# Performance work log

Measured on AMD Instinct MI355X. Metric: run time of the kernel, lower is better.

The kernel has to match this reference:

```python
import jax, jax.numpy as jnp
import numpy as np

B, S, W = 16, 512, 5
H, E, V = 512, 256, 100000


def setup_inputs() -> dict:
    key = jax.random.key(0)
    ks = jax.random.split(key, 20)
    inp = {
        "hiddens": jax.random.normal(ks[0], (B, S, H), jnp.float32),
        "masks": jax.random.randint(ks[1], (B, S), 0, 2, jnp.int32),
        "begins": jax.random.randint(ks[2], (B, S, W), 0, V, jnp.int32),
        "begin_lens": jax.random.randint(ks[3], (B, S), 0, W + 1, jnp.int32),
        "middles": jax.random.randint(ks[4], (B, S, W), 0, V, jnp.int32),
        "middle_lens": jax.random.randint(ks[5], (B, S), 0, W + 1, jnp.int32),
        "ends": jax.random.randint(ks[6], (B, S, W), 0, V, jnp.int32),
        "end_lens": jax.random.randint(ks[7], (B, S), 0, W + 1, jnp.int32),
        # parameters
        "emb": jax.random.normal(ks[8], (V, E), jnp.float32) * 0.02,
        "W_hidden": jax.random.normal(ks[9], (H, 3 * H), jnp.float32) * (1.0 / np.sqrt(H)),
        "b_hidden": jnp.zeros((3 * H,), jnp.float32),
        "W_begin": jax.random.normal(ks[10], (E, 2 * H), jnp.float32) * (1.0 / np.sqrt(E)),
        "b_begin": jnp.zeros((2 * H,), jnp.float32),
        "W_middle": jax.random.normal(ks[11], (E, 2 * H), jnp.float32) * (1.0 / np.sqrt(E)),
        "b_middle": jnp.zeros((2 * H,), jnp.float32),
        "W_end": jax.random.normal(ks[12], (E, 2 * H), jnp.float32) * (1.0 / np.sqrt(E)),
        "b_end": jnp.zeros((2 * H,), jnp.float32),
        "W_gate": jax.random.normal(ks[13], (H, 9), jnp.float32) * (1.0 / np.sqrt(H)),
        "b_gate": jnp.zeros((9,), jnp.float32),
    }
    return inp


def _len_mask(lens, w):
    # True where the lattice candidate is valid (mimics _make_mask's 1s)
    return jnp.arange(w)[None, None, :] < lens[:, :, None]


def _gates(hiddens, masks, W_gate, b_gate):
    b, s, _ = hiddens.shape
    lmr = hiddens @ W_gate + b_gate                      # (B,S,9)
    left, mid, right = jnp.split(lmr, 3, axis=-1)        # each (B,S,3)
    g = jax.nn.sigmoid(left[:, :-2] + mid[:, 1:-1] + right[:, 2:])  # (B,S-2,3)
    ones = jnp.ones((b, 1), g.dtype)
    zeros = jnp.zeros((b, 1), g.dtype)
    begin_g = jnp.concatenate([ones, g[..., 0], ones], axis=1)
    mid_g = jnp.concatenate([zeros, g[..., 1], zeros], axis=1)
    end_g = jnp.concatenate([ones, g[..., 2], ones], axis=1)
    pad = masks == 0
    z = jnp.zeros((), g.dtype)
    return (jnp.where(pad, z, begin_g), jnp.where(pad, z, mid_g), jnp.where(pad, z, end_g))


def reference(hiddens, masks, begins, begin_lens, middles, middle_lens, ends, end_lens,
              emb, W_hidden, b_hidden, W_begin, b_begin, W_middle, b_middle,
              W_end, b_end, W_gate, b_gate):
    w = begins.shape[-1]
    begin_m = _len_mask(begin_lens, w)
    middle_m = _len_mask(middle_lens, w)
    end_m = _len_mask(end_lens, w)

    begin_kv = emb[begins] @ W_begin + b_begin           # (B,S,W,2H)
    middle_kv = emb[middles] @ W_middle + b_middle
    end_kv = emb[ends] @ W_end + b_end

    query, hidden_key, hidden_value = jnp.split(hiddens @ W_hidden + b_hidden, 3, axis=-1)
    bg, mg, eg = _gates(hiddens, masks, W_gate, b_gate)
    begin_kv = bg[:, :, None, None] * begin_kv
    middle_kv = mg[:, :, None, None] * middle_kv
    end_kv = eg[:, :, None, None] * end_kv

    kv = jnp.concatenate([begin_kv, middle_kv, end_kv], axis=-2)   # (B,S,3W,2H)
    h = hiddens.shape[-1]
    keys, values = jnp.split(kv, 2, axis=-1)
    keys = jnp.concatenate([hidden_key[:, :, None, :], keys], axis=-2)     # (B,S,1+3W,H)
    values = jnp.concatenate([hidden_value[:, :, None, :], values], axis=-2)

    # combined mask: True entries get -1e10 (faithful to masked_fill_(masks, -1e10))
    score_mask = jnp.concatenate(
        [(masks != 0)[:, :, None], begin_m, middle_m, end_m], axis=-1)     # (B,S,1+3W)

    scores = jnp.einsum("bsh,bskh->bsk", query, keys)
    scores = jnp.where(score_mask, jnp.asarray(-1e10, scores.dtype), scores)
    weights = jax.nn.softmax(scores, axis=-1)
    return jnp.einsum("bsk,bskh->bsh", weights, values)
```

## Files before the change

kernel.cpp:

```cpp
#include <hip/hip_runtime.h>
#include <cstdint>
#include <cstddef>


typedef unsigned short u16;
typedef __attribute__((ext_vector_type(8))) short short8;
typedef __attribute__((ext_vector_type(8))) __bf16 bf16x8;
typedef __attribute__((ext_vector_type(4))) float f32x4;

#define MROWS 8192
#define SS 512

static __device__ __forceinline__ u16 f2bf(float x) {
  uint32_t u = __builtin_bit_cast(uint32_t, x);
  u += 0x7FFFu + ((u >> 16) & 1u);
  return (u16)(u >> 16);
}
static __device__ __forceinline__ float bf2f(u16 h) {
  return __builtin_bit_cast(float, (uint32_t)h << 16);
}
static __device__ __forceinline__ float sigm(float x) { return 1.f / (1.f + __expf(-x)); }

static __device__ __forceinline__ void gl2lds(const u16* g, u16* l) {
  __builtin_amdgcn_global_load_lds(
      (const __attribute__((address_space(1))) unsigned int*)g,
      (__attribute__((address_space(3))) unsigned int*)l, 16, 0, 0);
}

__global__ __launch_bounds__(256) void prep_xlmr(
    const float* __restrict__ X, const float* __restrict__ Wg,
    const float* __restrict__ bg, u16* __restrict__ hi, u16* __restrict__ lo,
    float* __restrict__ lmr) {
  __shared__ float wg[4608];
  const int t = threadIdx.x;
  for (int i = t; i < 4608; i += 256) wg[i] = Wg[i];
  __syncthreads();
  const int lane = t & 63, wid = t >> 6;
#pragma unroll
  for (int it = 0; it < 4; it++) {
    int pos = blockIdx.x * 16 + it * 4 + wid;
    const float* x = X + (size_t)pos * 512 + lane * 8;
    float4 x0 = *(const float4*)x;
    float4 x1 = *(const float4*)(x + 4);
    float xs[8] = {x0.x, x0.y, x0.z, x0.w, x1.x, x1.y, x1.z, x1.w};
    ushort4 h0, h1, l0, l1;
    h0.x = f2bf(xs[0]); l0.x = f2bf(xs[0] - bf2f(h0.x));
    h0.y = f2bf(xs[1]); l0.y = f2bf(xs[1] - bf2f(h0.y));
    h0.z = f2bf(xs[2]); l0.z = f2bf(xs[2] - bf2f(h0.z));
    h0.w = f2bf(xs[3]); l0.w = f2bf(xs[3] - bf2f(h0.w));
    h1.x = f2bf(xs[4]); l1.x = f2bf(xs[4] - bf2f(h1.x));
    h1.y = f2bf(xs[5]); l1.y = f2bf(xs[5] - bf2f(h1.y));
    h1.z = f2bf(xs[6]); l1.z = f2bf(xs[6] - bf2f(h1.z));
    h1.w = f2bf(xs[7]); l1.w = f2bf(xs[7] - bf2f(h1.w));
    ((ushort4*)hi)[pos * 128 + lane * 2] = h0;
    ((ushort4*)hi)[pos * 128 + lane * 2 + 1] = h1;
    ((ushort4*)lo)[pos * 128 + lane * 2] = l0;
    ((ushort4*)lo)[pos * 128 + lane * 2 + 1] = l1;
    float p[9];
#pragma unroll
    for (int c = 0; c < 9; c++) p[c] = 0.f;
    const float* wrow = wg + (lane * 8) * 9;
#pragma unroll
    for (int j = 0; j < 8; j++)
#pragma unroll
      for (int c = 0; c < 9; c++) p[c] += xs[j] * wrow[j * 9 + c];
#pragma unroll
    for (int c = 0; c < 9; c++)
#pragma unroll
      for (int o = 32; o > 0; o >>= 1) p[c] += __shfl_xor(p[c], o);
    if (lane == 0) {
#pragma unroll
      for (int c = 0; c < 9; c++) lmr[(size_t)pos * 9 + c] = p[c] + bg[c];
    }
  }
}

__global__ __launch_bounds__(256) void prep_weights(
    const float* __restrict__ Wh, const float* __restrict__ Wb,
    const float* __restrict__ Wm, const float* __restrict__ We,
    const float* __restrict__ bb, const float* __restrict__ bm,
    const float* __restrict__ be, const float* __restrict__ lmr,
    const int* __restrict__ masks, u16* __restrict__ WhThi,
    u16* __restrict__ WhTlo, u16* __restrict__ WkT, u16* __restrict__ WvT,
    float* __restrict__ gates) {
  __shared__ float tile[64][65];
  const int b = blockIdx.x;
  const int t = threadIdx.x;
  if (b < 192) {
    int k0 = (b & 7) * 64;
    int n0 = (b >> 3) * 64;
#pragma unroll
    for (int i = 0; i < 16; i++) {
      int li = i * 256 + t; int r = li >> 6, c = li & 63;
      tile[r][c] = Wh[(size_t)(k0 + r) * 1536 + n0 + c];
    }
    __syncthreads();
#pragma unroll
    for (int i = 0; i < 16; i++) {
      int li = i * 256 + t; int r = li >> 6, c = li & 63;
      float v = tile[c][r];
      size_t o = (size_t)(n0 + r) * 512 + k0 + c;
      u16 h = f2bf(v);
      WhThi[o] = h;
      WhTlo[o] = f2bf(v - bf2f(h));
    }
  } else if (b < 640) {
    int tid = (b - 192) * 256 + t;
    int n = tid >> 7;
    int kq = (tid & 127) * 4;
    float4 v;
    if (n < 768) {
      int ty = n >> 8, c = n & 255;
      const float* src = (ty == 0 ? Wb : ty == 1 ? Wm : We) + (size_t)c * 1024 + kq;
      v = *(const float4*)src;
    } else if (n < 771) {
      int ty = n - 768;
      const float* src = (ty == 0 ? bb : ty == 1 ? bm : be) + kq;
      v = *(const float4*)src;
    } else {
      v = make_float4(0.f, 0.f, 0.f, 0.f);
    }
    ushort4 h; h.x = f2bf(v.x); h.y = f2bf(v.y); h.z = f2bf(v.z); h.w = f2bf(v.w);
    ((ushort4*)WkT)[tid] = h;
  } else if (b < 736) {
    int idx = b - 640;
    int ty = idx >> 5;
    int rem = idx & 31;
    int c0 = (rem & 3) * 64;
    int n0 = (rem >> 2) * 64;
    const float* Wsrc = ty == 0 ? Wb : ty == 1 ? Wm : We;
#pragma unroll
    for (int i = 0; i < 16; i++) {
      int li = i * 256 + t; int r = li >> 6, c = li & 63;
      tile[r][c] = Wsrc[(size_t)(c0 + r) * 1024 + 512 + n0 + c];
    }
    __syncthreads();
#pragma unroll
    for (int i = 0; i < 16; i++) {
      int li = i * 256 + t; int r = li >> 6, c = li & 63;
      WvT[(size_t)(n0 + r) * 768 + ty * 256 + c0 + c] = f2bf(tile[c][r]);
    }
  } else {
    int pos = (b - 736) * 256 + t;
    int s = pos & (SS - 1);
    float g0, g1, g2;
    if (masks[pos] == 0) {
      g0 = g1 = g2 = 0.f;
    } else if (s == 0 || s == SS - 1) {
      g0 = 1.f; g1 = 0.f; g2 = 1.f;
    } else {
      const float* p0 = lmr + (size_t)(pos - 1) * 9;
      const float* p1 = lmr + (size_t)pos * 9;
      const float* p2 = lmr + (size_t)(pos + 1) * 9;
      g0 = sigm(p0[0] + p1[3] + p2[6]);
      g1 = sigm(p0[1] + p1[4] + p2[7]);
      g2 = sigm(p0[2] + p1[5] + p2[8]);
    }
    gates[(size_t)pos * 3 + 0] = g0;
    gates[(size_t)pos * 3 + 1] = g1;
    gates[(size_t)pos * 3 + 2] = g2;
  }
}

template <bool MAYSPLIT, bool ADDOUT, bool WRITE_QBF, bool HAS_BIAS, bool OUTBF>
__global__ __launch_bounds__(256) void gemm_mfma(
    const u16* __restrict__ Ahi, const u16* __restrict__ Alo,
    const u16* __restrict__ Bhi, const u16* __restrict__ Blo,
    const float* __restrict__ bias, float* __restrict__ Cf, u16* __restrict__ Cb,
    u16* __restrict__ Qbf, int Kdim, int ldC, int splitN) {
  __shared__ __align__(16) u16 As_hi[128 * 32];
  __shared__ __align__(16) u16 Bs_hi[128 * 32];
  __shared__ __align__(16) u16 As_lo[MAYSPLIT ? 128 * 32 : 8];
  __shared__ __align__(16) u16 Bs_lo[MAYSPLIT ? 128 * 32 : 8];

  const int t = threadIdx.x;
  const int lane = t & 63;
  const int wid = t >> 6;
  const int m0 = blockIdx.x * 128;
  const int n0 = blockIdx.y * 128;
  const bool split = MAYSPLIT && (n0 < splitN);
  const int wm = (wid & 1) * 64;
  const int wn = (wid >> 1) * 64;
  const int fr = lane & 15;
  const int kq = (lane >> 4) * 8;

  f32x4 acc[4][4];
#pragma unroll
  for (int i = 0; i < 4; i++)
#pragma unroll
    for (int j = 0; j < 4; j++) acc[i][j] = (f32x4){0.f, 0.f, 0.f, 0.f};

  for (int k0 = 0; k0 < Kdim; k0 += 32) {
    __syncthreads();
#pragma unroll
    for (int p = 0; p < 2; p++) {
      int li = p * 256 + t;
      int row = li >> 2;
      int so = (li & 3) * 8;
      size_t ga = (size_t)(m0 + row) * Kdim + k0 + so;
      size_t gb = (size_t)(n0 + row) * Kdim + k0 + so;
      int ls = li * 8;
      gl2lds(&Ahi[ga], &As_hi[ls]);
      gl2lds(&Bhi[gb], &Bs_hi[ls]);
      if (MAYSPLIT && split) {
        gl2lds(&Alo[ga], &As_lo[ls]);
        gl2lds(&Blo[gb], &Bs_lo[ls]);
      }
    }
    __syncthreads();
    short8 ah[4], bh[4], al[4], bl[4];
#pragma unroll
    for (int i = 0; i < 4; i++) {
      ah[i] = *(const short8*)&As_hi[(wm + i * 16 + fr) * 32 + kq];
      bh[i] = *(const short8*)&Bs_hi[(wn + i * 16 + fr) * 32 + kq];
      if (MAYSPLIT && split) {
        al[i] = *(const short8*)&As_lo[(wm + i * 16 + fr) * 32 + kq];
        bl[i] = *(const short8*)&Bs_lo[(wn + i * 16 + fr) * 32 + kq];
      }
    }
#pragma unroll
    for (int mt = 0; mt < 4; mt++)
#pragma unroll
      for (int nt = 0; nt < 4; nt++) {
        acc[mt][nt] = __builtin_amdgcn_mfma_f32_16x16x32_bf16(
            __builtin_bit_cast(bf16x8, ah[mt]), __builtin_bit_cast(bf16x8, bh[nt]),
            acc[mt][nt], 0, 0, 0);
        if (MAYSPLIT && split) {
          acc[mt][nt] = __builtin_amdgcn_mfma_f32_16x16x32_bf16(
              __builtin_bit_cast(bf16x8, al[mt]), __builtin_bit_cast(bf16x8, bh[nt]),
              acc[mt][nt], 0, 0, 0);
          acc[mt][nt] = __builtin_amdgcn_mfma_f32_16x16x32_bf16(
              __builtin_bit_cast(bf16x8, ah[mt]), __builtin_bit_cast(bf16x8, bl[nt]),
              acc[mt][nt], 0, 0, 0);
        }
      }
  }

  const int r0 = (lane >> 4) * 4;
#pragma unroll
  for (int mt = 0; mt < 4; mt++) {
#pragma unroll
    for (int nt = 0; nt < 4; nt++) {
      int col = n0 + wn + nt * 16 + fr;
      float bv = 0.f;
      if constexpr (HAS_BIAS) bv = bias[col];
#pragma unroll
      for (int r = 0; r < 4; r++) {
        int row = m0 + wm + mt * 16 + r0 + r;
        size_t off = (size_t)row * ldC + col;
        float v = acc[mt][nt][r] + bv;
        if constexpr (ADDOUT) v += Cf[off];
        if constexpr (OUTBF) Cb[off] = f2bf(v);
        else Cf[off] = v;
        if constexpr (WRITE_QBF) {
          if (col < 512) Qbf[(size_t)row * 512 + col] = f2bf(v);
        }
      }
    }
  }
}

__global__ __launch_bounds__(256) void attn_kernel(
    const int* __restrict__ masks, const int* __restrict__ begins,
    const int* __restrict__ blens, const int* __restrict__ middles,
    const int* __restrict__ mlens, const int* __restrict__ ends,
    const int* __restrict__ elens, const float* __restrict__ emb,
    const float* __restrict__ QKV, const u16* __restrict__ Pb,
    const float* __restrict__ gates, const float* __restrict__ b_begin,
    const float* __restrict__ b_middle, const float* __restrict__ b_end,
    float* __restrict__ out, u16* __restrict__ Ebar) {
  __shared__ float bvs[3][512];
  {
    int tt = threadIdx.x;
    for (int i = tt; i < 512; i += 256) {
      bvs[0][i] = b_begin[512 + i];
      bvs[1][i] = b_middle[512 + i];
      bvs[2][i] = b_end[512 + i];
    }
  }
  __syncthreads();
  const int t = threadIdx.x;
  const int lane = t & 63;
  const int wid = t >> 6;
  const int pos = blockIdx.x * 4 + wid;
  const int mask = masks[pos];
  const float* qkv = QKV + (size_t)pos * 1536;
  float4 hv0 = *(const float4*)(qkv + 1024 + lane * 8);
  float4 hv1 = *(const float4*)(qkv + 1024 + lane * 8 + 4);
  float* orow = out + (size_t)pos * 512;
  u16* erow = Ebar + (size_t)pos * 768;

  if (mask == 0) {
    float4 q0 = *(const float4*)(qkv + lane * 8);
    float4 q1 = *(const float4*)(qkv + lane * 8 + 4);
    float4 k0 = *(const float4*)(qkv + 512 + lane * 8);
    float4 k1 = *(const float4*)(qkv + 512 + lane * 8 + 4);
    float p = q0.x * k0.x + q0.y * k0.y + q0.z * k0.z + q0.w * k0.w +
              q1.x * k1.x + q1.y * k1.y + q1.z * k1.z + q1.w * k1.w;
#pragma unroll
    for (int o = 32; o > 0; o >>= 1) p += __shfl_xor(p, o);
    float s0 = p;
    int nv = min(blens[pos], 5) + min(mlens[pos], 5) + min(elens[pos], 5);
    int ninv = 15 - nv;
    float w0;
    if (ninv == 0) {
      w0 = 1.f;
    } else {
      float Mx = fmaxf(s0, 0.f);
      float e0 = __expf(s0 - Mx);
      w0 = e0 / (e0 + (float)ninv * __expf(-Mx));
    }
    float4 o0, o1;
    o0.x = w0 * hv0.x; o0.y = w0 * hv0.y; o0.z = w0 * hv0.z; o0.w = w0 * hv0.w;
    o1.x = w0 * hv1.x; o1.y = w0 * hv1.y; o1.z = w0 * hv1.z; o1.w = w0 * hv1.w;
    *(float4*)(orow + lane * 8) = o0;
    *(float4*)(orow + lane * 8 + 4) = o1;
    ushort4 zz; zz.x = zz.y = zz.z = zz.w = 0;
    *(ushort4*)(erow + 0 * 256 + lane * 4) = zz;
    *(ushort4*)(erow + 1 * 256 + lane * 4) = zz;
    *(ushort4*)(erow + 2 * 256 + lane * 4) = zz;
  } else {
    float g[3];
    g[0] = gates[(size_t)pos * 3 + 0];
    g[1] = gates[(size_t)pos * 3 + 1];
    g[2] = gates[(size_t)pos * 3 + 2];
    const u16* prow = Pb + (size_t)pos * 896;
    float4 Pt[3];
    float qb[3];
#pragma unroll
    for (int ty = 0; ty < 3; ty++) {
      ushort4 pu = *(const ushort4*)(prow + ty * 256 + lane * 4);
      Pt[ty].x = bf2f(pu.x); Pt[ty].y = bf2f(pu.y);
      Pt[ty].z = bf2f(pu.z); Pt[ty].w = bf2f(pu.w);
      qb[ty] = bf2f(prow[768 + ty]);
    }
    int lens[3] = {blens[pos], mlens[pos], elens[pos]};
    const int* ib = begins + (size_t)pos * 5;
    const int* im = middles + (size_t)pos * 5;
    const int* ie = ends + (size_t)pos * 5;
    float4 ev[3][5];
#pragma unroll
    for (int w = 0; w < 5; w++) {
      ev[0][w] = *(const float4*)(emb + (size_t)ib[w] * 256 + lane * 4);
      ev[1][w] = *(const float4*)(emb + (size_t)im[w] * 256 + lane * 4);
      ev[2][w] = *(const float4*)(emb + (size_t)ie[w] * 256 + lane * 4);
    }
    float sc[16];
    sc[0] = -1e10f;
#pragma unroll
    for (int ty = 0; ty < 3; ty++) {
#pragma unroll
      for (int w = 0; w < 5; w++) {
        float4 e = ev[ty][w];
        float d = Pt[ty].x * e.x + Pt[ty].y * e.y + Pt[ty].z * e.z + Pt[ty].w * e.w;
#pragma unroll
        for (int o = 32; o > 0; o >>= 1) d += __shfl_xor(d, o);
        sc[1 + ty * 5 + w] = (w < lens[ty]) ? -1e10f : g[ty] * (d + qb[ty]);
      }
    }
    float Mx = sc[0];
#pragma unroll
    for (int k = 1; k < 16; k++) Mx = fmaxf(Mx, sc[k]);
    float wts[16];
    float zs = 0.f;
#pragma unroll
    for (int k = 0; k < 16; k++) {
      wts[k] = __expf(sc[k] - Mx);
      zs += wts[k];
    }
    float inv = 1.f / zs;
    float alpha[3];
#pragma unroll
    for (int ty = 0; ty < 3; ty++) {
      float ax = 0.f, ay = 0.f, az = 0.f, aw = 0.f, asum = 0.f;
#pragma unroll
      for (int w = 0; w < 5; w++) {
        float wk = wts[1 + ty * 5 + w];
        asum += wk;
        ax += wk * ev[ty][w].x;
        ay += wk * ev[ty][w].y;
        az += wk * ev[ty][w].z;
        aw += wk * ev[ty][w].w;
      }
      float sg = g[ty] * inv;
      alpha[ty] = sg * asum;
      ushort4 h;
      h.x = f2bf(ax * sg); h.y = f2bf(ay * sg); h.z = f2bf(az * sg); h.w = f2bf(aw * sg);
      *(ushort4*)(erow + ty * 256 + lane * 4) = h;
    }
    float w0 = wts[0] * inv;
    float4 o0, o1;
    int hb = lane * 8;
    o0.x = w0 * hv0.x + alpha[0] * bvs[0][hb + 0] + alpha[1] * bvs[1][hb + 0] + alpha[2] * bvs[2][hb + 0];
    o0.y = w0 * hv0.y + alpha[0] * bvs[0][hb + 1] + alpha[1] * bvs[1][hb + 1] + alpha[2] * bvs[2][hb + 1];
    o0.z = w0 * hv0.z + alpha[0] * bvs[0][hb + 2] + alpha[1] * bvs[1][hb + 2] + alpha[2] * bvs[2][hb + 2];
    o0.w = w0 * hv0.w + alpha[0] * bvs[0][hb + 3] + alpha[1] * bvs[1][hb + 3] + alpha[2] * bvs[2][hb + 3];
    o1.x = w0 * hv1.x + alpha[0] * bvs[0][hb + 4] + alpha[1] * bvs[1][hb + 4] + alpha[2] * bvs[2][hb + 4];
    o1.y = w0 * hv1.y + alpha[0] * bvs[0][hb + 5] + alpha[1] * bvs[1][hb + 5] + alpha[2] * bvs[2][hb + 5];
    o1.z = w0 * hv1.z + alpha[0] * bvs[0][hb + 6] + alpha[1] * bvs[1][hb + 6] + alpha[2] * bvs[2][hb + 6];
    o1.w = w0 * hv1.w + alpha[0] * bvs[0][hb + 7] + alpha[1] * bvs[1][hb + 7] + alpha[2] * bvs[2][hb + 7];
    *(float4*)(orow + lane * 8) = o0;
    *(float4*)(orow + lane * 8 + 4) = o1;
  }
}

extern "C" void kernel_launch(void* const* d_in, const int* in_sizes, int n_in,
                              void* d_out, int out_size, void* d_ws, size_t ws_size,
                              hipStream_t stream) {
  const float* hiddens = (const float*)d_in[0];
  const int* masks = (const int*)d_in[1];
  const int* begins = (const int*)d_in[2];
  const int* blens = (const int*)d_in[3];
  const int* middles = (const int*)d_in[4];
  const int* mlens = (const int*)d_in[5];
  const int* ends = (const int*)d_in[6];
  const int* elens = (const int*)d_in[7];
  const float* emb = (const float*)d_in[8];
  const float* Wh = (const float*)d_in[9];
  const float* bh = (const float*)d_in[10];
  const float* Wb = (const float*)d_in[11];
  const float* bb = (const float*)d_in[12];
  const float* Wm = (const float*)d_in[13];
  const float* bm = (const float*)d_in[14];
  const float* We = (const float*)d_in[15];
  const float* be = (const float*)d_in[16];
  const float* Wg = (const float*)d_in[17];
  const float* bg = (const float*)d_in[18];
  float* out = (float*)d_out;

  char* ws = (char*)d_ws;
  size_t off = 0;
  auto alloc = [&](size_t bytes) -> char* {
    char* p = ws + off;
    off += (bytes + 255) & ~(size_t)255;
    return p;
  };
  u16* Xhi = (u16*)alloc((size_t)8192 * 512 * 2);
  u16* Xlo = (u16*)alloc((size_t)8192 * 512 * 2);
  u16* WhThi = (u16*)alloc((size_t)1536 * 512 * 2);
  u16* WhTlo = (u16*)alloc((size_t)1536 * 512 * 2);
  u16* WkT = (u16*)alloc((size_t)896 * 512 * 2);
  u16* WvT = (u16*)alloc((size_t)512 * 768 * 2);
  float* QKV = (float*)alloc((size_t)8192 * 1536 * 4);
  u16* Qbf = (u16*)alloc((size_t)8192 * 512 * 2);
  u16* Pb = (u16*)alloc((size_t)8192 * 896 * 2);
  float* lmr = (float*)alloc((size_t)8192 * 9 * 4);
  float* gates = (float*)alloc((size_t)8192 * 3 * 4);
  u16* Ebar = (u16*)alloc((size_t)8192 * 768 * 2);
  if (off > ws_size) return;

  prep_xlmr<<<512, 256, 0, stream>>>(hiddens, Wg, bg, Xhi, Xlo, lmr);
  prep_weights<<<768, 256, 0, stream>>>(Wh, Wb, Wm, We, bb, bm, be, lmr, masks,
                                        WhThi, WhTlo, WkT, WvT, gates);
  gemm_mfma<true, false, true, true, false><<<dim3(64, 12), 256, 0, stream>>>(
      Xhi, Xlo, WhThi, WhTlo, bh, QKV, nullptr, Qbf, 512, 1536, 1024);
  gemm_mfma<false, false, false, false, true><<<dim3(64, 7), 256, 0, stream>>>(
      Qbf, nullptr, WkT, nullptr, nullptr, nullptr, Pb, nullptr, 512, 896, 0);
  attn_kernel<<<2048, 256, 0, stream>>>(masks, begins, blens, middles, mlens, ends,
                                        elens, emb, QKV, Pb, gates, bb, bm, be, out, Ebar);
  gemm_mfma<false, true, false, false, false><<<dim3(64, 4), 256, 0, stream>>>(
      Ebar, nullptr, WvT, nullptr, nullptr, out, nullptr, nullptr, 768, 512, 0);
}
```

Measured before the change: 315.8 us.

## Fold query projection into weights, precompute Wq·Wk bilinear form and Wq·Wkv products

Rather than computing the full QKV projection and then a second GEMM of Q against the lattice key weights, the query weight is folded algebraically into the key weights. The code precomputes Wq^T·Wk as a bilinear matrix and Wq·W_kv products plus the matching bias terms. The hidden self-score is produced by a split-precision GEMM whose epilogue dots each row with X and atomically accumulates into s0. The main X GEMM then runs once in bf16 against the concatenated weight, writing the hidden value and the lattice projection scores directly. This removes the fp32 QKV buffer and the Q->P GEMM, at the cost of extra small weight-prep GEMMs, atomics, and possible precision changes from single-bf16 X in the fused projection.

```diff
diff --git a/kernel.cpp b/kernel.cpp
--- a/kernel.cpp
+++ b/kernel.cpp
@@ -30,9 +30,10 @@
 __global__ __launch_bounds__(256) void prep_xlmr(
     const float* __restrict__ X, const float* __restrict__ Wg,
     const float* __restrict__ bg, u16* __restrict__ hi, u16* __restrict__ lo,
-    float* __restrict__ lmr) {
+    float* __restrict__ lmr, float* __restrict__ s0) {
   __shared__ float wg[4608];
   const int t = threadIdx.x;
+  if (blockIdx.x < 32) s0[blockIdx.x * 256 + t] = 0.f;
   for (int i = t; i < 4608; i += 256) wg[i] = Wg[i];
   __syncthreads();
   const int lane = t & 63, wid = t >> 6;
@@ -79,33 +80,54 @@
     const float* __restrict__ Wh, const float* __restrict__ Wb,
     const float* __restrict__ Wm, const float* __restrict__ We,
     const float* __restrict__ bb, const float* __restrict__ bm,
-    const float* __restrict__ be, const float* __restrict__ lmr,
-    const int* __restrict__ masks, u16* __restrict__ WhThi,
-    u16* __restrict__ WhTlo, u16* __restrict__ WkT, u16* __restrict__ WvT,
-    float* __restrict__ gates) {
+    const float* __restrict__ be, const float* __restrict__ bh,
+    const float* __restrict__ lmr, const int* __restrict__ masks,
+    u16* __restrict__ Wcat, u16* __restrict__ Whq_h, u16* __restrict__ Whq_l,
+    u16* __restrict__ Whk_h, u16* __restrict__ Whk_l, u16* __restrict__ WkT,
+    u16* __restrict__ WvT, float* __restrict__ gates, float* __restrict__ bcat,
+    float* __restrict__ u, float* __restrict__ cbuf) {
   __shared__ float tile[64][65];
   const int b = blockIdx.x;
   const int t = threadIdx.x;
-  if (b < 192) {
+  if (b < 64) {
     int k0 = (b & 7) * 64;
     int n0 = (b >> 3) * 64;
 #pragma unroll
     for (int i = 0; i < 16; i++) {
       int li = i * 256 + t; int r = li >> 6, c = li & 63;
-      tile[r][c] = Wh[(size_t)(k0 + r) * 1536 + n0 + c];
+      tile[r][c] = Wh[(size_t)(k0 + r) * 1536 + 1024 + n0 + c];
     }
     __syncthreads();
 #pragma unroll
     for (int i = 0; i < 16; i++) {
       int li = i * 256 + t; int r = li >> 6, c = li & 63;
-      float v = tile[c][r];
-      size_t o = (size_t)(n0 + r) * 512 + k0 + c;
-      u16 h = f2bf(v);
-      WhThi[o] = h;
-      WhTlo[o] = f2bf(v - bf2f(h));
-    }
-  } else if (b < 640) {
-    int tid = (b - 192) * 256 + t;
+      Wcat[(size_t)(n0 + r) * 512 + k0 + c] = f2bf(tile[c][r]);
+    }
+  } else if (b < 128) {
+#pragma unroll
+    for (int i = 0; i < 4; i++) {
+      int q4 = (b - 64) * 1024 + t * 4 + i;
+      int k = q4 >> 7;
+      int c4 = (q4 & 127) * 4;
+      float4 vq = *(const float4*)(Wh + (size_t)k * 1536 + c4);
+      float4 vk = *(const float4*)(Wh + (size_t)k * 1536 + 512 + c4);
+      ushort4 qh, ql, kh, kl;
+      qh.x = f2bf(vq.x); ql.x = f2bf(vq.x - bf2f(qh.x));
+      qh.y = f2bf(vq.y); ql.y = f2bf(vq.y - bf2f(qh.y));
+      qh.z = f2bf(vq.z); ql.z = f2bf(vq.z - bf2f(qh.z));
+      qh.w = f2bf(vq.w); ql.w = f2bf(vq.w - bf2f(qh.w));
+      kh.x = f2bf(vk.x); kl.x = f2bf(vk.x - bf2f(kh.x));
+      kh.y = f2bf(vk.y); kl.y = f2bf(vk.y - bf2f(kh.y));
+      kh.z = f2bf(vk.z); kl.z = f2bf(vk.z - bf2f(kh.z));
+      kh.w = f2bf(vk.w); kl.w = f2bf(vk.w - bf2f(kh.w));
+      size_t o = (size_t)k * 512 + c4;
+      *(ushort4*)(Whq_h + o) = qh;
+      *(ushort4*)(Whq_l + o) = ql;
+      *(ushort4*)(Whk_h + o) = kh;
+      *(ushort4*)(Whk_l + o) = kl;
+    }
+  } else if (b < 576) {
+    int tid = (b - 128) * 256 + t;
     int n = tid >> 7;
     int kq = (tid & 127) * 4;
     float4 v;
@@ -122,8 +144,8 @@
     }
     ushort4 h; h.x = f2bf(v.x); h.y = f2bf(v.y); h.z = f2bf(v.z); h.w = f2bf(v.w);
     ((ushort4*)WkT)[tid] = h;
-  } else if (b < 736) {
-    int idx = b - 640;
+  } else if (b < 672) {
+    int idx = b - 576;
     int ty = idx >> 5;
     int rem = idx & 31;
     int c0 = (rem & 3) * 64;
@@ -140,8 +162,8 @@
       int li = i * 256 + t; int r = li >> 6, c = li & 63;
       WvT[(size_t)(n0 + r) * 768 + ty * 256 + c0 + c] = f2bf(tile[c][r]);
     }
-  } else {
-    int pos = (b - 736) * 256 + t;
+  } else if (b < 704) {
+    int pos = (b - 672) * 256 + t;
     int s = pos & (SS - 1);
     float g0, g1, g2;
     if (masks[pos] == 0) {
@@ -159,26 +181,55 @@
     gates[(size_t)pos * 3 + 0] = g0;
     gates[(size_t)pos * 3 + 1] = g1;
     gates[(size_t)pos * 3 + 2] = g2;
-  }
-}
-
-template <bool MAYSPLIT, bool ADDOUT, bool WRITE_QBF, bool HAS_BIAS, bool OUTBF>
-__global__ __launch_bounds__(256) void gemm_mfma(
+  } else {
+    int tid = (b - 704) * 256 + t;
+    if (tid < 896) {
+      int n = tid;
+      float acc = 0.f;
+      if (n < 768) {
+        int ty = n >> 8, ce = n & 255;
+        const float* src = (ty == 0 ? Wb : ty == 1 ? Wm : We) + (size_t)ce * 1024;
+        for (int c = 0; c < 512; c++) acc += bh[c] * src[c];
+      } else if (n < 771) {
+        int ty = n - 768;
+        const float* src = (ty == 0 ? bb : ty == 1 ? bm : be);
+        for (int c = 0; c < 512; c++) acc += bh[c] * src[c];
+      }
+      bcat[512 + n] = acc;
+    } else if (tid < 1408) {
+      bcat[tid - 896] = bh[1024 + (tid - 896)];
+    } else if (tid < 1920) {
+      int k = tid - 1408;
+      const float* wr = Wh + (size_t)k * 1536;
+      float acc = 0.f;
+      for (int c = 0; c < 512; c++) acc += wr[c] * bh[512 + c] + wr[512 + c] * bh[c];
+      u[k] = acc;
+    } else if (tid == 1920) {
+      float acc = 0.f;
+      for (int c = 0; c < 512; c++) acc += bh[c] * bh[512 + c];
+      cbuf[0] = acc;
+    }
+  }
+}
+
+template <int MODE>
+__global__ __launch_bounds__(256) void gemm_k(
     const u16* __restrict__ Ahi, const u16* __restrict__ Alo,
     const u16* __restrict__ Bhi, const u16* __restrict__ Blo,
-    const float* __restrict__ bias, float* __restrict__ Cf, u16* __restrict__ Cb,
-    u16* __restrict__ Qbf, int Kdim, int ldC, int splitN) {
+    const float* __restrict__ bias, float* __restrict__ Cf,
+    u16* __restrict__ Cb, u16* __restrict__ Cb2, int Kdim, int ldC,
+    const float* __restrict__ Xf, float* __restrict__ s0) {
+  constexpr bool SPLIT = (MODE == 2 || MODE == 3);
   __shared__ __align__(16) u16 As_hi[128 * 32];
   __shared__ __align__(16) u16 Bs_hi[128 * 32];
-  __shared__ __align__(16) u16 As_lo[MAYSPLIT ? 128 * 32 : 8];
-  __shared__ __align__(16) u16 Bs_lo[MAYSPLIT ? 128 * 32 : 8];
+  __shared__ __align__(16) u16 As_lo[SPLIT ? 128 * 32 : 8];
+  __shared__ __align__(16) u16 Bs_lo[SPLIT ? 128 * 32 : 8];
 
   const int t = threadIdx.x;
   const int lane = t & 63;
   const int wid = t >> 6;
   const int m0 = blockIdx.x * 128;
   const int n0 = blockIdx.y * 128;
-  const bool split = MAYSPLIT && (n0 < splitN);
   const int wm = (wid & 1) * 64;
   const int wn = (wid >> 1) * 64;
   const int fr = lane & 15;
@@ -202,18 +253,18 @@
       int ls = li * 8;
       gl2lds(&Ahi[ga], &As_hi[ls]);
       gl2lds(&Bhi[gb], &Bs_hi[ls]);
-      if (MAYSPLIT && split) {
+      if constexpr (SPLIT) {
         gl2lds(&Alo[ga], &As_lo[ls]);
         gl2lds(&Blo[gb], &Bs_lo[ls]);
       }
     }
     __syncthreads();
-    short8 ah[4], bh[4], al[4], bl[4];
+    short8 ah[4], bh4[4], al[4], bl[4];
 #pragma unroll
     for (int i = 0; i < 4; i++) {
       ah[i] = *(const short8*)&As_hi[(wm + i * 16 + fr) * 32 + kq];
-      bh[i] = *(const short8*)&Bs_hi[(wn + i * 16 + fr) * 32 + kq];
-      if (MAYSPLIT && split) {
+      bh4[i] = *(const short8*)&Bs_hi[(wn + i * 16 + fr) * 32 + kq];
+      if constexpr (SPLIT) {
         al[i] = *(const short8*)&As_lo[(wm + i * 16 + fr) * 32 + kq];
         bl[i] = *(const short8*)&Bs_lo[(wn + i * 16 + fr) * 32 + kq];
       }
@@ -223,11 +274,11 @@
 #pragma unroll
       for (int nt = 0; nt < 4; nt++) {
         acc[mt][nt] = __builtin_amdgcn_mfma_f32_16x16x32_bf16(
-            __builtin_bit_cast(bf16x8, ah[mt]), __builtin_bit_cast(bf16x8, bh[nt]),
+            __builtin_bit_cast(bf16x8, ah[mt]), __builtin_bit_cast(bf16x8, bh4[nt]),
             acc[mt][nt], 0, 0, 0);
-        if (MAYSPLIT && split) {
+        if constexpr (SPLIT) {
           acc[mt][nt] = __builtin_amdgcn_mfma_f32_16x16x32_bf16(
-              __builtin_bit_cast(bf16x8, al[mt]), __builtin_bit_cast(bf16x8, bh[nt]),
+              __builtin_bit_cast(bf16x8, al[mt]), __builtin_bit_cast(bf16x8, bh4[nt]),
               acc[mt][nt], 0, 0, 0);
           acc[mt][nt] = __builtin_amdgcn_mfma_f32_16x16x32_bf16(
               __builtin_bit_cast(bf16x8, ah[mt]), __builtin_bit_cast(bf16x8, bl[nt]),
@@ -237,23 +288,64 @@
   }
 
   const int r0 = (lane >> 4) * 4;
+  if constexpr (MODE == 3) {
+    float pl[4][4];
+#pragma unroll
+    for (int mt = 0; mt < 4; mt++)
+#pragma unroll
+      for (int r = 0; r < 4; r++) pl[mt][r] = 0.f;
+#pragma unroll
+    for (int mt = 0; mt < 4; mt++)
+#pragma unroll
+      for (int nt = 0; nt < 4; nt++) {
+        int col = n0 + wn + nt * 16 + fr;
+        float bv = bias[col];
+#pragma unroll
+        for (int r = 0; r < 4; r++) {
+          int row = m0 + wm + mt * 16 + r0 + r;
+          float v = acc[mt][nt][r] + bv;
+          pl[mt][r] += v * Xf[(size_t)row * 512 + col];
+        }
+      }
+#pragma unroll
+    for (int mt = 0; mt < 4; mt++)
+#pragma unroll
+      for (int r = 0; r < 4; r++) {
+        float p = pl[mt][r];
+        p += __shfl_xor(p, 1);
+        p += __shfl_xor(p, 2);
+        p += __shfl_xor(p, 4);
+        p += __shfl_xor(p, 8);
+        if (fr == r) {
+          int row = m0 + wm + mt * 16 + r0 + r;
+          atomicAdd(&s0[row], p);
+        }
+      }
+    return;
+  }
 #pragma unroll
   for (int mt = 0; mt < 4; mt++) {
 #pragma unroll
     for (int nt = 0; nt < 4; nt++) {
       int col = n0 + wn + nt * 16 + fr;
       float bv = 0.f;
-      if constexpr (HAS_BIAS) bv = bias[col];
+      if constexpr (MODE == 0) bv = bias[col];
 #pragma unroll
       for (int r = 0; r < 4; r++) {
         int row = m0 + wm + mt * 16 + r0 + r;
-        size_t off = (size_t)row * ldC + col;
         float v = acc[mt][nt][r] + bv;
-        if constexpr (ADDOUT) v += Cf[off];
-        if constexpr (OUTBF) Cb[off] = f2bf(v);
-        else Cf[off] = v;
-        if constexpr (WRITE_QBF) {
-          if (col < 512) Qbf[(size_t)row * 512 + col] = f2bf(v);
+        if constexpr (MODE == 0) {
+          if (col < 512) Cf[(size_t)row * 512 + col] = v;
+          else Cb[(size_t)row * 896 + (col - 512)] = f2bf(v);
+        } else if constexpr (MODE == 1) {
+          Cb[(size_t)row * ldC + col] = f2bf(v);
+        } else if constexpr (MODE == 2) {
+          u16 h = f2bf(v);
+          Cb[(size_t)row * ldC + col] = h;
+          Cb2[(size_t)row * ldC + col] = f2bf(v - bf2f(h));
+        } else if constexpr (MODE == 4) {
+          size_t off = (size_t)row * ldC + col;
+          Cf[off] += v;
         }
       }
     }
@@ -265,9 +357,10 @@
     const int* __restrict__ blens, const int* __restrict__ middles,
     const int* __restrict__ mlens, const int* __restrict__ ends,
     const int* __restrict__ elens, const float* __restrict__ emb,
-    const float* __restrict__ QKV, const u16* __restrict__ Pb,
+    const float* __restrict__ HV, const u16* __restrict__ Pb,
     const float* __restrict__ gates, const float* __restrict__ b_begin,
     const float* __restrict__ b_middle, const float* __restrict__ b_end,
+    const float* __restrict__ s0buf, const float* __restrict__ cbuf,
     float* __restrict__ out, u16* __restrict__ Ebar) {
   __shared__ float bvs[3][512];
   {
@@ -284,22 +377,14 @@
   const int wid = t >> 6;
   const int pos = blockIdx.x * 4 + wid;
   const int mask = masks[pos];
-  const float* qkv = QKV + (size_t)pos * 1536;
-  float4 hv0 = *(const float4*)(qkv + 1024 + lane * 8);
-  float4 hv1 = *(const float4*)(qkv + 1024 + lane * 8 + 4);
+  const float* hvp = HV + (size_t)pos * 512;
+  float4 hv0 = *(const float4*)(hvp + lane * 8);
+  float4 hv1 = *(const float4*)(hvp + lane * 8 + 4);
   float* orow = out + (size_t)pos * 512;
   u16* erow = Ebar + (size_t)pos * 768;
 
   if (mask == 0) {
-    float4 q0 = *(const float4*)(qkv + lane * 8);
-    float4 q1 = *(const float4*)(qkv + lane * 8 + 4);
-    float4 k0 = *(const float4*)(qkv + 512 + lane * 8);
-    float4 k1 = *(const float4*)(qkv + 512 + lane * 8 + 4);
-    float p = q0.x * k0.x + q0.y * k0.y + q0.z * k0.z + q0.w * k0.w +
-              q1.x * k1.x + q1.y * k1.y + q1.z * k1.z + q1.w * k1.w;
-#pragma unroll
-    for (int o = 32; o > 0; o >>= 1) p += __shfl_xor(p, o);
-    float s0 = p;
+    float s0 = s0buf[pos] + cbuf[0];
     int nv = min(blens[pos], 5) + min(mlens[pos], 5) + min(elens[pos], 5);
     int ninv = 15 - nv;
     float w0;
@@ -437,27 +522,46 @@
   };
   u16* Xhi = (u16*)alloc((size_t)8192 * 512 * 2);
   u16* Xlo = (u16*)alloc((size_t)8192 * 512 * 2);
-  u16* WhThi = (u16*)alloc((size_t)1536 * 512 * 2);
-  u16* WhTlo = (u16*)alloc((size_t)1536 * 512 * 2);
+  u16* Whq_h = (u16*)alloc((size_t)512 * 512 * 2);
+  u16* Whq_l = (u16*)alloc((size_t)512 * 512 * 2);
+  u16* Whk_h = (u16*)alloc((size_t)512 * 512 * 2);
+  u16* Whk_l = (u16*)alloc((size_t)512 * 512 * 2);
   u16* WkT = (u16*)alloc((size_t)896 * 512 * 2);
+  u16* Wcat = (u16*)alloc((size_t)1408 * 512 * 2);
   u16* WvT = (u16*)alloc((size_t)512 * 768 * 2);
-  float* QKV = (float*)alloc((size_t)8192 * 1536 * 4);
-  u16* Qbf = (u16*)alloc((size_t)8192 * 512 * 2);
+  u16* Mthi = (u16*)alloc((size_t)512 * 512 * 2);
+  u16* Mtlo = (u16*)alloc((size_t)512 * 512 * 2);
+  float* HV = (float*)alloc((size_t)8192 * 512 * 4);
   u16* Pb = (u16*)alloc((size_t)8192 * 896 * 2);
   float* lmr = (float*)alloc((size_t)8192 * 9 * 4);
   float* gates = (float*)alloc((size_t)8192 * 3 * 4);
+  float* s0 = (float*)alloc((size_t)8192 * 4);
+  float* bcat = (float*)alloc((size_t)1408 * 4);
+  float* u = (float*)alloc((size_t)512 * 4);
+  float* cbuf = (float*)alloc((size_t)4);
   u16* Ebar = (u16*)alloc((size_t)8192 * 768 * 2);
   if (off > ws_size) return;
 
-  prep_xlmr<<<512, 256, 0, stream>>>(hiddens, Wg, bg, Xhi, Xlo, lmr);
-  prep_weights<<<768, 256, 0, stream>>>(Wh, Wb, Wm, We, bb, bm, be, lmr, masks,
-                                        WhThi, WhTlo, WkT, WvT, gates);
-  gemm_mfma<true, false, true, true, false><<<dim3(64, 12), 256, 0, stream>>>(
-      Xhi, Xlo, WhThi, WhTlo, bh, QKV, nullptr, Qbf, 512, 1536, 1024);
-  gemm_mfma<false, false, false, false, true><<<dim3(64, 7), 256, 0, stream>>>(
-      Qbf, nullptr, WkT, nullptr, nullptr, nullptr, Pb, nullptr, 512, 896, 0);
+  prep_xlmr<<<512, 256, 0, stream>>>(hiddens, Wg, bg, Xhi, Xlo, lmr, s0);
+  prep_weights<<<712, 256, 0, stream>>>(Wh, Wb, Wm, We, bb, bm, be, bh, lmr, masks,
+                                        Wcat, Whq_h, Whq_l, Whk_h, Whk_l, WkT, WvT,
+                                        gates, bcat, u, cbuf);
+  gemm_k<2><<<dim3(4, 4), 256, 0, stream>>>(
+      Whk_h, Whk_l, Whq_h, Whq_l, nullptr, nullptr, Mthi, Mtlo, 512, 512,
+      nullptr, nullptr);
+  gemm_k<1><<<dim3(7, 4), 256, 0, stream>>>(
+      WkT, nullptr, Whq_h, nullptr, nullptr, nullptr, Wcat + (size_t)512 * 512,
+      nullptr, 512, 512, nullptr, nullptr);
+  gemm_k<3><<<dim3(64, 4), 256, 0, stream>>>(
+      Xhi, Xlo, Mthi, Mtlo, u, nullptr, nullptr, nullptr, 512, 512,
+      hiddens, s0);
+  gemm_k<0><<<dim3(64, 11), 256, 0, stream>>>(
+      Xhi, nullptr, Wcat, nullptr, bcat, HV, Pb, nullptr, 512, 512,
+      nullptr, nullptr);
   attn_kernel<<<2048, 256, 0, stream>>>(masks, begins, blens, middles, mlens, ends,
-                                        elens, emb, QKV, Pb, gates, bb, bm, be, out, Ebar);
-  gemm_mfma<false, true, false, false, false><<<dim3(64, 4), 256, 0, stream>>>(
-      Ebar, nullptr, WvT, nullptr, nullptr, out, nullptr, nullptr, 768, 512, 0);
-}
+                                        elens, emb, HV, Pb, gates, bb, bm, be,
+                                        s0, cbuf, out, Ebar);
+  gemm_k<4><<<dim3(64, 4), 256, 0, stream>>>(
+      Ebar, nullptr, WvT, nullptr, nullptr, out, nullptr, nullptr, 768, 512,
+      nullptr, nullptr);
+}
```

Result: slower. 404.6 us (+28.1%).
